# Kernel optimization log

Measured on AMD Instinct MI355X. Metric: run time of the kernel, lower is better.

## Reference

```python
import jax, jax.numpy as jnp
import numpy as np

B, S, H = 1, 2048, 1024
NH, NKV, HD = 16, 4, 64
I, E, K = 2816, 8, 2
WIN = 512
EPS = 1e-5


def setup_inputs() -> dict:
    key = jax.random.key(0)
    ks = jax.random.split(key, 8)
    sd = 0.02
    return {
        "hidden_states": jax.random.normal(ks[0], (B, S, H), jnp.float32),
        "positions": jnp.arange(S, dtype=jnp.int64),
        "w_qkv": jax.random.normal(ks[1], ((NH + 2 * NKV) * HD, H), jnp.float32) * sd,
        "w_o": jax.random.normal(ks[2], (H, NH * HD), jnp.float32) * sd,
        "router_w": jax.random.normal(ks[3], (E, H), jnp.float32) * sd,
        "ws": jax.random.normal(ks[4], (E, 2 * I, H), jnp.float32) * sd,
        "w2s": jax.random.normal(ks[5], (E, H, I), jnp.float32) * sd,
        "ln1_w": jnp.ones((H,), jnp.float32),
        "ln2_w": jnp.ones((H,), jnp.float32),
    }


def _rmsnorm(x, w):
    return x * jax.lax.rsqrt(jnp.mean(x * x, axis=-1, keepdims=True) + EPS) * w


def reference(hidden_states, positions, w_qkv, w_o, router_w, ws, w2s, ln1_w, ln2_w):
    # residual is None on entry -> residual = input, then input_layernorm
    residual = hidden_states
    x = _rmsnorm(hidden_states, ln1_w)

    # qkv projection (torch Linear: y = x @ W.T), GQA split
    qkv = jnp.einsum("bsh,oh->bso", x, w_qkv)
    q_size, kv_size = NH * HD, NKV * HD
    q = qkv[..., :q_size].reshape(B, S, NH, HD)
    k = qkv[..., q_size:q_size + kv_size].reshape(B, S, NKV, HD)
    v = qkv[..., q_size + kv_size:].reshape(B, S, NKV, HD)
    rep = NH // NKV
    k = jnp.repeat(k, rep, axis=2)  # [B,S,NH,HD]
    v = jnp.repeat(v, rep, axis=2)

    scale = HD ** -0.5
    scores = jnp.einsum("bqhd,bkhd->bhqk", q, k) * scale
    i = jnp.arange(S)[:, None]
    j = jnp.arange(S)[None, :]
    mask = (j <= i) & ((i - j) < WIN)  # causal sliding window
    scores = jnp.where(mask, scores, jnp.finfo(scores.dtype).min)
    attn = jax.nn.softmax(scores, axis=-1)
    o = jnp.einsum("bhqk,bkhd->bqhd", attn, v).reshape(B, S, NH * HD)
    attn_out = jnp.einsum("bso,ho->bsh", o, w_o)

    # pre_moe_layernorm with residual: x += residual; residual = x; x = norm(x)
    x2 = attn_out + residual
    residual2 = x2
    h = _rmsnorm(x2, ln2_w)

    # MoE: router softmax, top-k (renormalize=False), per-expert SwiGLU FFN
    t = h.reshape(-1, H)  # [T,H]
    logits = jnp.einsum("th,eh->te", t, router_w)
    probs = jax.nn.softmax(logits, axis=-1)
    vals, idx = jax.lax.top_k(probs, K)  # [T,K]
    w_dense = jnp.sum(vals[:, :, None] * jax.nn.one_hot(idx, E, dtype=t.dtype), axis=1)  # [T,E]

    out = jnp.zeros_like(t)
    for e in range(E):
        gu = jnp.einsum("th,ih->ti", t, ws[e])  # [T,2I]
        g, u = gu[:, :I], gu[:, I:]
        a = jax.nn.silu(g) * u
        y = jnp.einsum("ti,hi->th", a, w2s[e])
        out = out + w_dense[:, e:e + 1] * y

    return out.reshape(B, S, H), residual2
```

## Files before the change

kernel.cpp:

```cpp
#include <hip/hip_runtime.h>
#include <stdint.h>

typedef unsigned short u16;
typedef __attribute__((ext_vector_type(8))) short short8;
typedef __attribute__((ext_vector_type(4))) float f32x4;

constexpr int SEQ   = 2048;
constexpr int HID   = 1024;
constexpr int NHEAD = 16;
constexpr int QKVD  = 1536;
constexpr int FFI   = 2816;
constexpr int NEXP  = 8;
constexpr int WINSZ = 512;
#define EPSF 1e-5f

__device__ __forceinline__ float bf2f(u16 u) {
  union { unsigned int i; float f; } v; v.i = ((unsigned int)u) << 16; return v.f;
}
__device__ __forceinline__ u16 f2bf(float f) {
  union { unsigned int i; float f; } v; v.f = f;
  unsigned int i = v.i;
  return (u16)((i + 0x7fffu + ((i >> 16) & 1u)) >> 16);
}

__device__ __forceinline__ void gload_lds16(const void* g, void* l) {
  __builtin_amdgcn_global_load_lds((__attribute__((address_space(1))) void*)g,
                                   (__attribute__((address_space(3))) void*)l,
                                   16, 0, 0);
}

#define MFMA_BF16(a, b, c) __builtin_amdgcn_mfma_f32_16x16x32_bf16(a, b, c, 0, 0, 0)

constexpr int CN1 = QKVD * HID / 4;
constexpr int CN2 = HID * HID / 4;
constexpr int CN3 = NEXP * 2 * FFI * HID / 4;
constexpr int CN4 = NEXP * HID * FFI / 4;
constexpr int CN_SMALL = CN1 + CN2;
constexpr int CN_BIG   = CN3 + CN4;
constexpr int NCONV_BLK = CN_BIG / 1024;
constexpr int NATTN_BLK = (SEQ / 64) * NHEAD;

__global__ __launch_bounds__(256) void k_f2b_small(
    const float* __restrict__ wqkv, const float* __restrict__ wo,
    u16* __restrict__ dq, u16* __restrict__ dwo) {
  int j = (blockIdx.x * 256 + threadIdx.x) * 4;
#pragma unroll
  for (int t = 0; t < 4; ++t, ++j) {
    if (j >= CN_SMALL) return;
    const float* s; u16* d; int i = j;
    if (i < CN1) { s = wqkv; d = dq; } else { i -= CN1; s = wo; d = dwo; }
    float4 v = ((const float4*)s)[i];
    ushort4 o;
    o.x = f2bf(v.x); o.y = f2bf(v.y); o.z = f2bf(v.z); o.w = f2bf(v.w);
    ((ushort4*)d)[i] = o;
  }
}

__global__ __launch_bounds__(256) void k_rmsnorm(const float* __restrict__ x,
                                                 const float* __restrict__ w,
                                                 u16* __restrict__ y) {
  const int tkn = blockIdx.x, tid = threadIdx.x, wid = tid >> 6, lane = tid & 63;
  const float* xr = x + (size_t)tkn * HID;
  float4 v = *(const float4*)&xr[tid * 4];
  float ss = v.x * v.x + v.y * v.y + v.z * v.z + v.w * v.w;
#pragma unroll
  for (int m = 1; m < 64; m <<= 1) ss += __shfl_xor(ss, m);
  __shared__ float red[4];
  if (lane == 0) red[wid] = ss;
  __syncthreads();
  ss = red[0] + red[1] + red[2] + red[3];
  float sc = rsqrtf(ss * (1.0f / HID) + EPSF);
  float4 wv = *(const float4*)&w[tid * 4];
  ushort4 o;
  o.x = f2bf(v.x * sc * wv.x);
  o.y = f2bf(v.y * sc * wv.y);
  o.z = f2bf(v.z * sc * wv.z);
  o.w = f2bf(v.w * sc * wv.w);
  *(ushort4*)&y[(size_t)tkn * HID + tid * 4] = o;
}

__global__ __launch_bounds__(256, 2) void k_gemm_bt_sk(
    const u16* __restrict__ A, const u16* __restrict__ B, float* __restrict__ Cf,
    int N, int K, int Kc) {
  __shared__ u16 As[128 * 64];
  __shared__ u16 Bs[128 * 64];
  const int tid = threadIdx.x, wid = tid >> 6, lane = tid & 63;
  const int quad = lane >> 4, l16 = lane & 15;
  const int wr = wid >> 1, wc = wid & 1;
  const int m0 = blockIdx.y * 128, n0 = blockIdx.x * 128;
  const int M = gridDim.y * 128;
  const int kbase = blockIdx.z * Kc;
  const int sr = lane >> 3, sc = (lane & 7) * 8;
  f32x4 acc[4][4] = {};
  const int KT = Kc >> 6;
  for (int kt = 0; kt < KT; ++kt) {
    const int k0 = kbase + (kt << 6);
#pragma unroll
    for (int it = 0; it < 4; ++it) {
      int seg = wid * 4 + it;
      int row = seg * 8 + sr;
      gload_lds16(&A[(size_t)(m0 + row) * K + k0 + sc], &As[seg * 512]);
      gload_lds16(&B[(size_t)(n0 + row) * K + k0 + sc], &Bs[seg * 512]);
    }
    __syncthreads();
#pragma unroll
    for (int ks = 0; ks < 2; ++ks) {
      short8 af[4], bf[4];
#pragma unroll
      for (int t = 0; t < 4; ++t)
        af[t] = *(const short8*)&As[(64 * wr + 16 * t + l16) * 64 + ks * 32 + quad * 8];
#pragma unroll
      for (int t = 0; t < 4; ++t)
        bf[t] = *(const short8*)&Bs[(64 * wc + 16 * t + l16) * 64 + ks * 32 + quad * 8];
#pragma unroll
      for (int mt = 0; mt < 4; ++mt)
#pragma unroll
        for (int nt = 0; nt < 4; ++nt)
          acc[mt][nt] = MFMA_BF16(af[mt], bf[nt], acc[mt][nt]);
    }
    __syncthreads();
  }
  float* Co = Cf + (size_t)blockIdx.z * M * N;
#pragma unroll
  for (int mt = 0; mt < 4; ++mt)
#pragma unroll
    for (int r = 0; r < 4; ++r) {
      int row = m0 + 64 * wr + 16 * mt + quad * 4 + r;
#pragma unroll
      for (int nt = 0; nt < 4; ++nt) {
        int col = n0 + 64 * wc + 16 * nt + l16;
        Co[(size_t)row * N + col] = acc[mt][nt][r];
      }
    }
}

__global__ __launch_bounds__(256) void k_sum2_bf16(const float* __restrict__ a,
                                                   const float* __restrict__ b,
                                                   u16* __restrict__ o, int n4) {
  int i = blockIdx.x * 256 + threadIdx.x;
  if (i >= n4) return;
  float4 x = ((const float4*)a)[i];
  float4 y = ((const float4*)b)[i];
  ushort4 u;
  u.x = f2bf(x.x + y.x); u.y = f2bf(x.y + y.y);
  u.z = f2bf(x.z + y.z); u.w = f2bf(x.w + y.w);
  ((ushort4*)o)[i] = u;
}

__global__ __launch_bounds__(256, 2) void k_attn_conv(
    const u16* __restrict__ qkv, u16* __restrict__ o,
    const float* __restrict__ ws, const float* __restrict__ w2s,
    u16* __restrict__ dws, u16* __restrict__ dw2) {
  const int bid = blockIdx.x;
  const int tid = threadIdx.x;
  if (bid >= NATTN_BLK) {
    int j = (bid - NATTN_BLK) * 1024 + tid * 4;
    const float* s; u16* d;
    if (j < CN3) { s = ws; d = dws; } else { j -= CN3; s = w2s; d = dw2; }
    float4 v0 = ((const float4*)s)[j + 0];
    float4 v1 = ((const float4*)s)[j + 1];
    float4 v2 = ((const float4*)s)[j + 2];
    float4 v3 = ((const float4*)s)[j + 3];
    ushort4 o0, o1, o2, o3;
    o0.x = f2bf(v0.x); o0.y = f2bf(v0.y); o0.z = f2bf(v0.z); o0.w = f2bf(v0.w);
    o1.x = f2bf(v1.x); o1.y = f2bf(v1.y); o1.z = f2bf(v1.z); o1.w = f2bf(v1.w);
    o2.x = f2bf(v2.x); o2.y = f2bf(v2.y); o2.z = f2bf(v2.z); o2.w = f2bf(v2.w);
    o3.x = f2bf(v3.x); o3.y = f2bf(v3.y); o3.z = f2bf(v3.z); o3.w = f2bf(v3.w);
    ((ushort4*)d)[j + 0] = o0;
    ((ushort4*)d)[j + 1] = o1;
    ((ushort4*)d)[j + 2] = o2;
    ((ushort4*)d)[j + 3] = o3;
    return;
  }
  const int qb = bid & 31;
  const int h  = bid >> 5;
  const int q0 = qb * 64;
  const int g = h >> 2;
  __shared__ u16 Qs[64 * 72], Ks[64 * 72], Vt[64 * 72], Ps[64 * 72];
  const int wid = tid >> 6, lane = tid & 63;
  const int quad = lane >> 4, l16 = lane & 15;

#pragma unroll
  for (int it = 0; it < 2; ++it) {
    int idx = it * 256 + tid;
    int row = idx >> 3, c8 = (idx & 7) * 8;
    *(short8*)&Qs[row * 72 + c8] =
        *(const short8*)&qkv[(size_t)(q0 + row) * QKVD + h * 64 + c8];
  }

  f32x4 oacc[4] = {};
  float mrun[4], lrun[4];
#pragma unroll
  for (int r = 0; r < 4; ++r) { mrun[r] = -1e30f; lrun[r] = 0.f; }

  const int ktlo = (q0 >= WINSZ) ? ((q0 - WINSZ + 1) >> 6) : 0;
  const int kthi = qb;
  for (int kt = ktlo; kt <= kthi; ++kt) {
#pragma unroll
    for (int it = 0; it < 2; ++it) {
      int idx = it * 256 + tid;
      int row = idx >> 3, c8 = (idx & 7) * 8;
      *(short8*)&Ks[row * 72 + c8] =
          *(const short8*)&qkv[(size_t)(kt * 64 + row) * QKVD + 1024 + g * 64 + c8];
    }
#pragma unroll
    for (int it = 0; it < 8; ++it) {
      int idx = it * 256 + tid;
      int key = idx >> 5;
      int d = (idx & 31) * 2;
      unsigned int u = *(const unsigned int*)&qkv[(size_t)(kt * 64 + key) * QKVD + 1280 + g * 64 + d];
      Vt[d * 72 + key] = (u16)(u & 0xffffu);
      Vt[(d + 1) * 72 + key] = (u16)(u >> 16);
    }
    __syncthreads();

    f32x4 sa[4] = {};
#pragma unroll
    for (int ks = 0; ks < 2; ++ks) {
      short8 af = *(const short8*)&Qs[(16 * wid + l16) * 72 + ks * 32 + quad * 8];
#pragma unroll
      for (int ct = 0; ct < 4; ++ct) {
        short8 bf = *(const short8*)&Ks[(16 * ct + l16) * 72 + ks * 32 + quad * 8];
        sa[ct] = MFMA_BF16(af, bf, sa[ct]);
      }
    }

    float pvv[4][4];
#pragma unroll
    for (int r = 0; r < 4; ++r) {
      int i = q0 + 16 * wid + quad * 4 + r;
      float mx = -1e30f;
#pragma unroll
      for (int ct = 0; ct < 4; ++ct) {
        int j = kt * 64 + 16 * ct + l16;
        float v = sa[ct][r] * 0.125f;
        bool ok = (j <= i) && (i - j < WINSZ);
        v = ok ? v : -1e30f;
        pvv[ct][r] = v;
        mx = fmaxf(mx, v);
      }
#pragma unroll
      for (int m = 1; m < 16; m <<= 1) mx = fmaxf(mx, __shfl_xor(mx, m));
      float mnew = fmaxf(mrun[r], mx);
      float alpha = __expf(mrun[r] - mnew);
      float s = 0.f;
#pragma unroll
      for (int ct = 0; ct < 4; ++ct) {
        float p = (pvv[ct][r] > -1e29f) ? __expf(pvv[ct][r] - mnew) : 0.f;
        pvv[ct][r] = p;
        s += p;
      }
#pragma unroll
      for (int m = 1; m < 16; m <<= 1) s += __shfl_xor(s, m);
      lrun[r] = lrun[r] * alpha + s;
      mrun[r] = mnew;
#pragma unroll
      for (int ct = 0; ct < 4; ++ct) oacc[ct][r] *= alpha;
    }
#pragma unroll
    for (int ct = 0; ct < 4; ++ct)
#pragma unroll
      for (int r = 0; r < 4; ++r)
        Ps[(16 * wid + quad * 4 + r) * 72 + 16 * ct + l16] = f2bf(pvv[ct][r]);
    __syncthreads();

#pragma unroll
    for (int ks = 0; ks < 2; ++ks) {
      short8 af = *(const short8*)&Ps[(16 * wid + l16) * 72 + ks * 32 + quad * 8];
#pragma unroll
      for (int ct = 0; ct < 4; ++ct) {
        short8 bf = *(const short8*)&Vt[(16 * ct + l16) * 72 + ks * 32 + quad * 8];
        oacc[ct] = MFMA_BF16(af, bf, oacc[ct]);
      }
    }
    __syncthreads();
  }

#pragma unroll
  for (int ct = 0; ct < 4; ++ct)
#pragma unroll
    for (int r = 0; r < 4; ++r) {
      int row = q0 + 16 * wid + quad * 4 + r;
      float v = oacc[ct][r] / lrun[r];
      o[(size_t)row * HID + h * 64 + 16 * ct + l16] = f2bf(v);
    }
}

__global__ __launch_bounds__(256) void k_rms2_router(
    const float* __restrict__ o0, const float* __restrict__ o1,
    const float* __restrict__ hs, const float* __restrict__ ln2,
    const float* __restrict__ rw, float* __restrict__ out1,
    u16* __restrict__ T, int* __restrict__ counts,
    int* __restrict__ tok_idx, float* __restrict__ tok_w) {
  const int tkn = blockIdx.x, tid = threadIdx.x, wid = tid >> 6, lane = tid & 63;
  const size_t base = (size_t)tkn * HID + tid * 4;
  float4 a = *(const float4*)&o0[base];
  float4 b = *(const float4*)&o1[base];
  float4 h = *(const float4*)&hs[base];
  float4 v;
  v.x = a.x + b.x + h.x; v.y = a.y + b.y + h.y;
  v.z = a.z + b.z + h.z; v.w = a.w + b.w + h.w;
  *(float4*)&out1[base] = v;
  float ss = v.x * v.x + v.y * v.y + v.z * v.z + v.w * v.w;
#pragma unroll
  for (int m = 1; m < 64; m <<= 1) ss += __shfl_xor(ss, m);
  __shared__ float red[4];
  if (lane == 0) red[wid] = ss;
  __syncthreads();
  ss = red[0] + red[1] + red[2] + red[3];
  float sc = rsqrtf(ss * (1.0f / HID) + EPSF);
  float4 lw = *(const float4*)&ln2[tid * 4];
  float t0 = v.x * sc * lw.x;
  float t1 = v.y * sc * lw.y;
  float t2 = v.z * sc * lw.z;
  float t3 = v.w * sc * lw.w;
  ushort4 o;
  o.x = f2bf(t0); o.y = f2bf(t1); o.z = f2bf(t2); o.w = f2bf(t3);
  *(ushort4*)&T[(size_t)tkn * HID + tid * 4] = o;

  float p[8];
#pragma unroll
  for (int e = 0; e < 8; ++e) {
    float4 r = *(const float4*)&rw[e * HID + tid * 4];
    p[e] = t0 * r.x + t1 * r.y + t2 * r.z + t3 * r.w;
  }
#pragma unroll
  for (int e = 0; e < 8; ++e)
#pragma unroll
    for (int m = 1; m < 64; m <<= 1) p[e] += __shfl_xor(p[e], m);
  __shared__ float pr[4][8];
  if (lane == 0)
#pragma unroll
    for (int e = 0; e < 8; ++e) pr[wid][e] = p[e];
  __syncthreads();
  if (tid == 0) {
    float lg[8];
#pragma unroll
    for (int e = 0; e < 8; ++e) lg[e] = pr[0][e] + pr[1][e] + pr[2][e] + pr[3][e];
    float mx = lg[0];
#pragma unroll
    for (int e = 1; e < 8; ++e) mx = fmaxf(mx, lg[e]);
    float ex[8], se = 0.f;
#pragma unroll
    for (int e = 0; e < 8; ++e) { ex[e] = __expf(lg[e] - mx); se += ex[e]; }
    int b0 = 0;
#pragma unroll
    for (int e = 1; e < 8; ++e) if (lg[e] > lg[b0]) b0 = e;
    int b1 = (b0 == 0) ? 1 : 0;
#pragma unroll
    for (int e = 0; e < 8; ++e) if (e != b0 && lg[e] > lg[b1]) b1 = e;
    float inv = 1.0f / se;
    int s0 = atomicAdd(&counts[b0], 1);
    tok_idx[b0 * SEQ + s0] = tkn;
    tok_w[b0 * SEQ + s0] = ex[b0] * inv;
    int s1 = atomicAdd(&counts[b1], 1);
    tok_idx[b1 * SEQ + s1] = tkn;
    tok_w[b1 * SEQ + s1] = ex[b1] * inv;
  }
}

__global__ void k_offsets(const int* __restrict__ counts, int* __restrict__ offs) {
  if (threadIdx.x == 0 && blockIdx.x == 0) {
    int s = 0;
    for (int e = 0; e < NEXP; ++e) { offs[e] = s; s += counts[e]; }
    offs[NEXP] = s;
  }
}

__global__ __launch_bounds__(256, 2) void k_moe_gu(
    const u16* __restrict__ T, const u16* __restrict__ Wgu,
    const int* __restrict__ counts, const int* __restrict__ offs,
    const int* __restrict__ tok_idx, u16* __restrict__ Abuf) {
  const int e = blockIdx.z;
  const int cnt = counts[e];
  const int m0 = blockIdx.y * 128;
  if (m0 >= cnt) return;
  const int n0 = blockIdx.x * 64;
  const u16* We = Wgu + (size_t)e * 2 * FFI * HID;
  const int* ti = tok_idx + e * SEQ;
  const int aoff = offs[e];
  __shared__ u16 As[128 * 64], Bg[64 * 64], Bu[64 * 64];
  const int tid = threadIdx.x, wid = tid >> 6, lane = tid & 63;
  const int quad = lane >> 4, l16 = lane & 15;
  const int wr = wid >> 1, wc = wid & 1;
  const int sr = lane >> 3, sc = (lane & 7) * 8;
  int tokrow[4];
#pragma unroll
  for (int it = 0; it < 4; ++it) {
    int row = (wid * 4 + it) * 8 + sr;
    int ra = m0 + row;
    if (ra > cnt - 1) ra = cnt - 1;
    tokrow[it] = ti[ra];
  }
  f32x4 accg[4][2] = {}, accu[4][2] = {};
  for (int kt = 0; kt < 16; ++kt) {
    const int k0 = kt << 6;
#pragma unroll
    for (int it = 0; it < 4; ++it) {
      int seg = wid * 4 + it;
      gload_lds16(&T[(size_t)tokrow[it] * HID + k0 + sc], &As[seg * 512]);
    }
#pragma unroll
    for (int it = 0; it < 2; ++it) {
      int seg = wid * 2 + it;
      int row = seg * 8 + sr;
      gload_lds16(&We[(size_t)(n0 + row) * HID + k0 + sc], &Bg[seg * 512]);
      gload_lds16(&We[(size_t)(FFI + n0 + row) * HID + k0 + sc], &Bu[seg * 512]);
    }
    __syncthreads();
#pragma unroll
    for (int ks = 0; ks < 2; ++ks) {
      short8 af[4], bg[2], bu[2];
#pragma unroll
      for (int t = 0; t < 4; ++t)
        af[t] = *(const short8*)&As[(64 * wr + 16 * t + l16) * 64 + ks * 32 + quad * 8];
#pragma unroll
      for (int t = 0; t < 2; ++t) {
        bg[t] = *(const short8*)&Bg[(32 * wc + 16 * t + l16) * 64 + ks * 32 + quad * 8];
        bu[t] = *(const short8*)&Bu[(32 * wc + 16 * t + l16) * 64 + ks * 32 + quad * 8];
      }
#pragma unroll
      for (int mt = 0; mt < 4; ++mt)
#pragma unroll
        for (int nt = 0; nt < 2; ++nt) {
          accg[mt][nt] = MFMA_BF16(af[mt], bg[nt], accg[mt][nt]);
          accu[mt][nt] = MFMA_BF16(af[mt], bu[nt], accu[mt][nt]);
        }
    }
    __syncthreads();
  }
#pragma unroll
  for (int mt = 0; mt < 4; ++mt)
#pragma unroll
    for (int r = 0; r < 4; ++r) {
      int rl = 64 * wr + 16 * mt + quad * 4 + r;
      int grow = m0 + rl;
      if (grow < cnt) {
        size_t rbase = (size_t)(aoff + grow) * FFI;
#pragma unroll
        for (int nt = 0; nt < 2; ++nt) {
          int col = n0 + 32 * wc + 16 * nt + l16;
          float gv = accg[mt][nt][r];
          float uv = accu[mt][nt][r];
          float a = gv / (1.0f + __expf(-gv)) * uv;
          Abuf[rbase + col] = f2bf(a);
        }
      }
    }
}

__global__ __launch_bounds__(256, 2) void k_moe_y(
    const u16* __restrict__ Abuf, const u16* __restrict__ W2,
    const int* __restrict__ counts, const int* __restrict__ offs,
    const int* __restrict__ tok_idx, const float* __restrict__ tok_w,
    float* __restrict__ outf) {
  const int e = blockIdx.z >> 2;
  const int sk = blockIdx.z & 3;
  const int cnt = counts[e];
  const int m0 = blockIdx.y * 128;
  if (m0 >= cnt) return;
  const int n0 = blockIdx.x * 128;
  const int kbase = sk * 704;
  const u16* We = W2 + (size_t)e * HID * FFI;
  const int aoff = offs[e];
  __shared__ u16 As[128 * 64], Bs[128 * 64];
  const int tid = threadIdx.x, wid = tid >> 6, lane = tid & 63;
  const int quad = lane >> 4, l16 = lane & 15;
  const int wr = wid >> 1, wc = wid & 1;
  const int sr = lane >> 3, sc = (lane & 7) * 8;
  int arow[4];
#pragma unroll
  for (int it = 0; it < 4; ++it) {
    int row = (wid * 4 + it) * 8 + sr;
    int ra = m0 + row;
    if (ra > cnt - 1) ra = cnt - 1;
    arow[it] = aoff + ra;
  }
  f32x4 acc[4][4] = {};
  for (int kt = 0; kt < 11; ++kt) {
    const int k0 = kbase + (kt << 6);
#pragma unroll
    for (int it = 0; it < 4; ++it) {
      int seg = wid * 4 + it;
      int row = seg * 8 + sr;
      gload_lds16(&Abuf[(size_t)arow[it] * FFI + k0 + sc], &As[seg * 512]);
      gload_lds16(&We[(size_t)(n0 + row) * FFI + k0 + sc], &Bs[seg * 512]);
    }
    __syncthreads();
#pragma unroll
    for (int ks = 0; ks < 2; ++ks) {
      short8 af[4], bf[4];
#pragma unroll
      for (int t = 0; t < 4; ++t)
        af[t] = *(const short8*)&As[(64 * wr + 16 * t + l16) * 64 + ks * 32 + quad * 8];
#pragma unroll
      for (int t = 0; t < 4; ++t)
        bf[t] = *(const short8*)&Bs[(64 * wc + 16 * t + l16) * 64 + ks * 32 + quad * 8];
#pragma unroll
      for (int mt = 0; mt < 4; ++mt)
#pragma unroll
        for (int nt = 0; nt < 4; ++nt)
          acc[mt][nt] = MFMA_BF16(af[mt], bf[nt], acc[mt][nt]);
    }
    __syncthreads();
  }
#pragma unroll
  for (int mt = 0; mt < 4; ++mt)
#pragma unroll
    for (int r = 0; r < 4; ++r) {
      int rl = 64 * wr + 16 * mt + quad * 4 + r;
      int grow = m0 + rl;
      if (grow < cnt) {
        int tok = tok_idx[e * SEQ + grow];
        float wgt = tok_w[e * SEQ + grow];
        size_t obase = (size_t)tok * HID;
#pragma unroll
        for (int nt = 0; nt < 4; ++nt) {
          int col = n0 + 64 * wc + 16 * nt + l16;
          atomicAdd(&outf[obase + col], wgt * acc[mt][nt][r]);
        }
      }
    }
}

extern "C" void kernel_launch(void* const* d_in, const int* in_sizes, int n_in,
                              void* d_out, int out_size, void* d_ws, size_t ws_size,
                              hipStream_t stream) {
  const float* hs   = (const float*)d_in[0];
  const float* wqkv = (const float*)d_in[2];
  const float* wo   = (const float*)d_in[3];
  const float* rwt  = (const float*)d_in[4];
  const float* wsx  = (const float*)d_in[5];
  const float* w2s  = (const float*)d_in[6];
  const float* ln1  = (const float*)d_in[7];
  const float* ln2  = (const float*)d_in[8];
  float* out0 = (float*)d_out;
  float* out1 = out0 + (size_t)SEQ * HID;

  char* p = (char*)d_ws;
  u16* xn      = (u16*)p;   p += (size_t)SEQ * HID * 2;
  u16* qkv     = (u16*)p;   p += (size_t)SEQ * QKVD * 2;
  u16* ob      = (u16*)p;   p += (size_t)SEQ * HID * 2;
  float* qkvf  = (float*)p; p += (size_t)2 * SEQ * QKVD * 4;
  int* counts  = (int*)p;   p += 32;
  int* offs    = (int*)p;   p += 64;
  int* tok_idx = (int*)p;   p += (size_t)NEXP * SEQ * 4;
  float* tok_w = (float*)p; p += (size_t)NEXP * SEQ * 4;
  u16* abuf    = (u16*)p;   p += (size_t)2 * SEQ * FFI * 2;
  u16* wqkv_b  = (u16*)p;   p += (size_t)QKVD * HID * 2;
  u16* wo_b    = (u16*)p;   p += (size_t)HID * HID * 2;
  u16* ws_b    = (u16*)p;   p += (size_t)NEXP * 2 * FFI * HID * 2;
  u16* w2s_b   = (u16*)p;   p += (size_t)NEXP * HID * FFI * 2;

  u16* tb      = xn;
  float* oacc0 = qkvf;
  float* oacc1 = qkvf + (size_t)SEQ * HID;

  hipMemsetAsync(counts, 0, 32, stream);
  hipMemsetAsync(out0, 0, (size_t)SEQ * HID * 4, stream);

  k_f2b_small<<<(CN_SMALL / 4 + 255) / 256, 256, 0, stream>>>(
      wqkv, wo, wqkv_b, wo_b);
  k_rmsnorm<<<SEQ, 256, 0, stream>>>(hs, ln1, xn);
  k_gemm_bt_sk<<<dim3(QKVD / 128, SEQ / 128, 2), 256, 0, stream>>>(
      xn, wqkv_b, qkvf, QKVD, HID, 512);
  k_sum2_bf16<<<(SEQ * QKVD / 4 + 255) / 256, 256, 0, stream>>>(
      qkvf, qkvf + (size_t)SEQ * QKVD, qkv, SEQ * QKVD / 4);
  k_attn_conv<<<NATTN_BLK + NCONV_BLK, 256, 0, stream>>>(
      qkv, ob, wsx, w2s, ws_b, w2s_b);
  k_gemm_bt_sk<<<dim3(HID / 128, SEQ / 128, 2), 256, 0, stream>>>(
      ob, wo_b, oacc0, HID, HID, 512);
  k_rms2_router<<<SEQ, 256, 0, stream>>>(oacc0, oacc1, hs, ln2, rwt, out1, tb,
                                         counts, tok_idx, tok_w);
  k_offsets<<<1, 64, 0, stream>>>(counts, offs);
  k_moe_gu<<<dim3(FFI / 64, SEQ / 128, NEXP), 256, 0, stream>>>(
      tb, ws_b, counts, offs, tok_idx, abuf);
  k_moe_y<<<dim3(HID / 128, SEQ / 128, NEXP * 4), 256, 0, stream>>>(
      abuf, w2s_b, counts, offs, tok_idx, tok_w, out0);
}
```

Baseline: 634.6 us.

## Double-buffer GEMM tiles, drop split-K for dense GEMMs, replace MoE atomics with gather

Fuses the first RMSNorm with the small weight conversion into one launch. The dense QKV and output-projection GEMMs drop split-K and the separate reduction kernel in favour of 128x64 tiles that write bf16 or fp32 directly. All GEMM kernels (dense, MoE gate/up, MoE down) now double-buffer their LDS tiles so global loads overlap MFMA work. The MoE down projection cuts split-K from 4 to 2, writes partials into a per-slot buffer, and a new gather kernel combines the two experts per token with their routing weights. This removes the output memset and the float atomics, at the cost of more LDS per block and an extra fp32 intermediate buffer plus one more launch.

```diff
diff --git a/kernel.cpp b/kernel.cpp
--- a/kernel.cpp
+++ b/kernel.cpp
@@ -14,9 +14,6 @@
 constexpr int WINSZ = 512;
 #define EPSF 1e-5f
 
-__device__ __forceinline__ float bf2f(u16 u) {
-  union { unsigned int i; float f; } v; v.i = ((unsigned int)u) << 16; return v.f;
-}
 __device__ __forceinline__ u16 f2bf(float f) {
   union { unsigned int i; float f; } v; v.f = f;
   unsigned int i = v.i;
@@ -40,14 +37,37 @@
 constexpr int NCONV_BLK = CN_BIG / 1024;
 constexpr int NATTN_BLK = (SEQ / 64) * NHEAD;
 
-__global__ __launch_bounds__(256) void k_f2b_small(
+__global__ __launch_bounds__(256) void k_prep(
+    const float* __restrict__ x, const float* __restrict__ w, u16* __restrict__ y,
     const float* __restrict__ wqkv, const float* __restrict__ wo,
     u16* __restrict__ dq, u16* __restrict__ dwo) {
-  int j = (blockIdx.x * 256 + threadIdx.x) * 4;
-#pragma unroll
-  for (int t = 0; t < 4; ++t, ++j) {
-    if (j >= CN_SMALL) return;
-    const float* s; u16* d; int i = j;
+  const int bid = blockIdx.x, tid = threadIdx.x;
+  __shared__ float red[4];
+  if (bid < SEQ) {
+    const int wid = tid >> 6, lane = tid & 63;
+    const float* xr = x + (size_t)bid * HID;
+    float4 v = *(const float4*)&xr[tid * 4];
+    float ss = v.x * v.x + v.y * v.y + v.z * v.z + v.w * v.w;
+#pragma unroll
+    for (int m = 1; m < 64; m <<= 1) ss += __shfl_xor(ss, m);
+    if (lane == 0) red[wid] = ss;
+    __syncthreads();
+    ss = red[0] + red[1] + red[2] + red[3];
+    float sc = rsqrtf(ss * (1.0f / HID) + EPSF);
+    float4 wv = *(const float4*)&w[tid * 4];
+    ushort4 o;
+    o.x = f2bf(v.x * sc * wv.x);
+    o.y = f2bf(v.y * sc * wv.y);
+    o.z = f2bf(v.z * sc * wv.z);
+    o.w = f2bf(v.w * sc * wv.w);
+    *(ushort4*)&y[(size_t)bid * HID + tid * 4] = o;
+    return;
+  }
+  int j = (bid - SEQ) * 1024 + tid;
+#pragma unroll
+  for (int t = 0; t < 4; ++t) {
+    int i = j + t * 256;
+    const float* s; u16* d;
     if (i < CN1) { s = wqkv; d = dq; } else { i -= CN1; s = wo; d = dwo; }
     float4 v = ((const float4*)s)[i];
     ushort4 o;
@@ -56,95 +76,84 @@
   }
 }
 
-__global__ __launch_bounds__(256) void k_rmsnorm(const float* __restrict__ x,
-                                                 const float* __restrict__ w,
-                                                 u16* __restrict__ y) {
-  const int tkn = blockIdx.x, tid = threadIdx.x, wid = tid >> 6, lane = tid & 63;
-  const float* xr = x + (size_t)tkn * HID;
-  float4 v = *(const float4*)&xr[tid * 4];
-  float ss = v.x * v.x + v.y * v.y + v.z * v.z + v.w * v.w;
-#pragma unroll
-  for (int m = 1; m < 64; m <<= 1) ss += __shfl_xor(ss, m);
-  __shared__ float red[4];
-  if (lane == 0) red[wid] = ss;
-  __syncthreads();
-  ss = red[0] + red[1] + red[2] + red[3];
-  float sc = rsqrtf(ss * (1.0f / HID) + EPSF);
-  float4 wv = *(const float4*)&w[tid * 4];
-  ushort4 o;
-  o.x = f2bf(v.x * sc * wv.x);
-  o.y = f2bf(v.y * sc * wv.y);
-  o.z = f2bf(v.z * sc * wv.z);
-  o.w = f2bf(v.w * sc * wv.w);
-  *(ushort4*)&y[(size_t)tkn * HID + tid * 4] = o;
-}
-
-__global__ __launch_bounds__(256, 2) void k_gemm_bt_sk(
-    const u16* __restrict__ A, const u16* __restrict__ B, float* __restrict__ Cf,
-    int N, int K, int Kc) {
-  __shared__ u16 As[128 * 64];
-  __shared__ u16 Bs[128 * 64];
+__global__ __launch_bounds__(256, 2) void k_gemm_bt(
+    const u16* __restrict__ A, const u16* __restrict__ B,
+    void* __restrict__ Cout, int N, int K, int wf32) {
+  __shared__ u16 As[2][128 * 64];
+  __shared__ u16 Bs[2][64 * 64];
   const int tid = threadIdx.x, wid = tid >> 6, lane = tid & 63;
   const int quad = lane >> 4, l16 = lane & 15;
   const int wr = wid >> 1, wc = wid & 1;
-  const int m0 = blockIdx.y * 128, n0 = blockIdx.x * 128;
-  const int M = gridDim.y * 128;
-  const int kbase = blockIdx.z * Kc;
+  const int m0 = blockIdx.y * 128, n0 = blockIdx.x * 64;
   const int sr = lane >> 3, sc = (lane & 7) * 8;
-  f32x4 acc[4][4] = {};
-  const int KT = Kc >> 6;
+  f32x4 acc[4][2] = {};
+  const int KT = K >> 6;
+
+#define GSTAGE(buf, k0)                                                          \
+  {                                                                              \
+    _Pragma("unroll") for (int it = 0; it < 4; ++it) {                           \
+      int seg = wid * 4 + it;                                                    \
+      int row = seg * 8 + sr;                                                    \
+      gload_lds16(&A[(size_t)(m0 + row) * K + (k0) + sc], &As[buf][seg * 512]);  \
+    }                                                                            \
+    _Pragma("unroll") for (int it = 0; it < 2; ++it) {                           \
+      int seg = wid * 2 + it;                                                    \
+      int row = seg * 8 + sr;                                                    \
+      gload_lds16(&B[(size_t)(n0 + row) * K + (k0) + sc], &Bs[buf][seg * 512]);  \
+    }                                                                            \
+  }
+
+  GSTAGE(0, 0);
+  __syncthreads();
+  int cur = 0;
   for (int kt = 0; kt < KT; ++kt) {
-    const int k0 = kbase + (kt << 6);
-#pragma unroll
-    for (int it = 0; it < 4; ++it) {
-      int seg = wid * 4 + it;
-      int row = seg * 8 + sr;
-      gload_lds16(&A[(size_t)(m0 + row) * K + k0 + sc], &As[seg * 512]);
-      gload_lds16(&B[(size_t)(n0 + row) * K + k0 + sc], &Bs[seg * 512]);
+    if (kt + 1 < KT) GSTAGE(cur ^ 1, (kt + 1) << 6);
+#pragma unroll
+    for (int ks = 0; ks < 2; ++ks) {
+      short8 af[4], bf[2];
+#pragma unroll
+      for (int t = 0; t < 4; ++t)
+        af[t] = *(const short8*)&As[cur][(64 * wr + 16 * t + l16) * 64 + ks * 32 + quad * 8];
+#pragma unroll
+      for (int t = 0; t < 2; ++t)
+        bf[t] = *(const short8*)&Bs[cur][(32 * wc + 16 * t + l16) * 64 + ks * 32 + quad * 8];
+#pragma unroll
+      for (int mt = 0; mt < 4; ++mt)
+#pragma unroll
+        for (int nt = 0; nt < 2; ++nt)
+          acc[mt][nt] = MFMA_BF16(af[mt], bf[nt], acc[mt][nt]);
     }
     __syncthreads();
-#pragma unroll
-    for (int ks = 0; ks < 2; ++ks) {
-      short8 af[4], bf[4];
-#pragma unroll
-      for (int t = 0; t < 4; ++t)
-        af[t] = *(const short8*)&As[(64 * wr + 16 * t + l16) * 64 + ks * 32 + quad * 8];
-#pragma unroll
-      for (int t = 0; t < 4; ++t)
-        bf[t] = *(const short8*)&Bs[(64 * wc + 16 * t + l16) * 64 + ks * 32 + quad * 8];
-#pragma unroll
-      for (int mt = 0; mt < 4; ++mt)
-#pragma unroll
-        for (int nt = 0; nt < 4; ++nt)
-          acc[mt][nt] = MFMA_BF16(af[mt], bf[nt], acc[mt][nt]);
-    }
-    __syncthreads();
-  }
-  float* Co = Cf + (size_t)blockIdx.z * M * N;
-#pragma unroll
-  for (int mt = 0; mt < 4; ++mt)
-#pragma unroll
-    for (int r = 0; r < 4; ++r) {
-      int row = m0 + 64 * wr + 16 * mt + quad * 4 + r;
-#pragma unroll
-      for (int nt = 0; nt < 4; ++nt) {
-        int col = n0 + 64 * wc + 16 * nt + l16;
-        Co[(size_t)row * N + col] = acc[mt][nt][r];
-      }
-    }
-}
-
-__global__ __launch_bounds__(256) void k_sum2_bf16(const float* __restrict__ a,
-                                                   const float* __restrict__ b,
-                                                   u16* __restrict__ o, int n4) {
-  int i = blockIdx.x * 256 + threadIdx.x;
-  if (i >= n4) return;
-  float4 x = ((const float4*)a)[i];
-  float4 y = ((const float4*)b)[i];
-  ushort4 u;
-  u.x = f2bf(x.x + y.x); u.y = f2bf(x.y + y.y);
-  u.z = f2bf(x.z + y.z); u.w = f2bf(x.w + y.w);
-  ((ushort4*)o)[i] = u;
+    cur ^= 1;
+  }
+#undef GSTAGE
+  if (wf32) {
+    float* C = (float*)Cout;
+#pragma unroll
+    for (int mt = 0; mt < 4; ++mt)
+#pragma unroll
+      for (int r = 0; r < 4; ++r) {
+        int row = m0 + 64 * wr + 16 * mt + quad * 4 + r;
+#pragma unroll
+        for (int nt = 0; nt < 2; ++nt) {
+          int col = n0 + 32 * wc + 16 * nt + l16;
+          C[(size_t)row * N + col] = acc[mt][nt][r];
+        }
+      }
+  } else {
+    u16* C = (u16*)Cout;
+#pragma unroll
+    for (int mt = 0; mt < 4; ++mt)
+#pragma unroll
+      for (int r = 0; r < 4; ++r) {
+        int row = m0 + 64 * wr + 16 * mt + quad * 4 + r;
+#pragma unroll
+        for (int nt = 0; nt < 2; ++nt) {
+          int col = n0 + 32 * wc + 16 * nt + l16;
+          C[(size_t)row * N + col] = f2bf(acc[mt][nt][r]);
+        }
+      }
+  }
 }
 
 __global__ __launch_bounds__(256, 2) void k_attn_conv(
@@ -154,22 +163,17 @@
   const int bid = blockIdx.x;
   const int tid = threadIdx.x;
   if (bid >= NATTN_BLK) {
-    int j = (bid - NATTN_BLK) * 1024 + tid * 4;
-    const float* s; u16* d;
-    if (j < CN3) { s = ws; d = dws; } else { j -= CN3; s = w2s; d = dw2; }
-    float4 v0 = ((const float4*)s)[j + 0];
-    float4 v1 = ((const float4*)s)[j + 1];
-    float4 v2 = ((const float4*)s)[j + 2];
-    float4 v3 = ((const float4*)s)[j + 3];
-    ushort4 o0, o1, o2, o3;
-    o0.x = f2bf(v0.x); o0.y = f2bf(v0.y); o0.z = f2bf(v0.z); o0.w = f2bf(v0.w);
-    o1.x = f2bf(v1.x); o1.y = f2bf(v1.y); o1.z = f2bf(v1.z); o1.w = f2bf(v1.w);
-    o2.x = f2bf(v2.x); o2.y = f2bf(v2.y); o2.z = f2bf(v2.z); o2.w = f2bf(v2.w);
-    o3.x = f2bf(v3.x); o3.y = f2bf(v3.y); o3.z = f2bf(v3.z); o3.w = f2bf(v3.w);
-    ((ushort4*)d)[j + 0] = o0;
-    ((ushort4*)d)[j + 1] = o1;
-    ((ushort4*)d)[j + 2] = o2;
-    ((ushort4*)d)[j + 3] = o3;
+    int j = (bid - NATTN_BLK) * 1024 + tid;
+#pragma unroll
+    for (int t = 0; t < 4; ++t) {
+      int i = j + t * 256;
+      const float* s; u16* d;
+      if (i < CN3) { s = ws; d = dws; } else { i -= CN3; s = w2s; d = dw2; }
+      float4 v = ((const float4*)s)[i];
+      ushort4 u;
+      u.x = f2bf(v.x); u.y = f2bf(v.y); u.z = f2bf(v.z); u.w = f2bf(v.w);
+      ((ushort4*)d)[i] = u;
+    }
     return;
   }
   const int qb = bid & 31;
@@ -287,19 +291,17 @@
 }
 
 __global__ __launch_bounds__(256) void k_rms2_router(
-    const float* __restrict__ o0, const float* __restrict__ o1,
-    const float* __restrict__ hs, const float* __restrict__ ln2,
-    const float* __restrict__ rw, float* __restrict__ out1,
-    u16* __restrict__ T, int* __restrict__ counts,
-    int* __restrict__ tok_idx, float* __restrict__ tok_w) {
+    const float* __restrict__ of, const float* __restrict__ hs,
+    const float* __restrict__ ln2, const float* __restrict__ rw,
+    float* __restrict__ out1, u16* __restrict__ T, int* __restrict__ counts,
+    int* __restrict__ tok_idx, int* __restrict__ tok_slot,
+    float* __restrict__ tok_pw) {
   const int tkn = blockIdx.x, tid = threadIdx.x, wid = tid >> 6, lane = tid & 63;
   const size_t base = (size_t)tkn * HID + tid * 4;
-  float4 a = *(const float4*)&o0[base];
-  float4 b = *(const float4*)&o1[base];
+  float4 a = *(const float4*)&of[base];
   float4 h = *(const float4*)&hs[base];
   float4 v;
-  v.x = a.x + b.x + h.x; v.y = a.y + b.y + h.y;
-  v.z = a.z + b.z + h.z; v.w = a.w + b.w + h.w;
+  v.x = a.x + h.x; v.y = a.y + h.y; v.z = a.z + h.z; v.w = a.w + h.w;
   *(float4*)&out1[base] = v;
   float ss = v.x * v.x + v.y * v.y + v.z * v.z + v.w * v.w;
 #pragma unroll
@@ -352,10 +354,12 @@
     float inv = 1.0f / se;
     int s0 = atomicAdd(&counts[b0], 1);
     tok_idx[b0 * SEQ + s0] = tkn;
-    tok_w[b0 * SEQ + s0] = ex[b0] * inv;
+    tok_slot[2 * tkn] = b0 * SEQ + s0;
+    tok_pw[2 * tkn] = ex[b0] * inv;
     int s1 = atomicAdd(&counts[b1], 1);
     tok_idx[b1 * SEQ + s1] = tkn;
-    tok_w[b1 * SEQ + s1] = ex[b1] * inv;
+    tok_slot[2 * tkn + 1] = b1 * SEQ + s1;
+    tok_pw[2 * tkn + 1] = ex[b1] * inv;
   }
 }
 
@@ -379,7 +383,7 @@
   const u16* We = Wgu + (size_t)e * 2 * FFI * HID;
   const int* ti = tok_idx + e * SEQ;
   const int aoff = offs[e];
-  __shared__ u16 As[128 * 64], Bg[64 * 64], Bu[64 * 64];
+  __shared__ u16 As[2][128 * 64], Bg[2][64 * 64], Bu[2][64 * 64];
   const int tid = threadIdx.x, wid = tid >> 6, lane = tid & 63;
   const int quad = lane >> 4, l16 = lane & 15;
   const int wr = wid >> 1, wc = wid & 1;
@@ -393,31 +397,37 @@
     tokrow[it] = ti[ra];
   }
   f32x4 accg[4][2] = {}, accu[4][2] = {};
+
+#define MSTAGE(buf, k0)                                                            \
+  {                                                                                \
+    _Pragma("unroll") for (int it = 0; it < 4; ++it) {                             \
+      int seg = wid * 4 + it;                                                      \
+      gload_lds16(&T[(size_t)tokrow[it] * HID + (k0) + sc], &As[buf][seg * 512]);  \
+    }                                                                              \
+    _Pragma("unroll") for (int it = 0; it < 2; ++it) {                             \
+      int seg = wid * 2 + it;                                                      \
+      int row = seg * 8 + sr;                                                      \
+      gload_lds16(&We[(size_t)(n0 + row) * HID + (k0) + sc], &Bg[buf][seg * 512]); \
+      gload_lds16(&We[(size_t)(FFI + n0 + row) * HID + (k0) + sc],                 \
+                  &Bu[buf][seg * 512]);                                            \
+    }                                                                              \
+  }
+
+  MSTAGE(0, 0);
+  __syncthreads();
+  int cur = 0;
   for (int kt = 0; kt < 16; ++kt) {
-    const int k0 = kt << 6;
-#pragma unroll
-    for (int it = 0; it < 4; ++it) {
-      int seg = wid * 4 + it;
-      gload_lds16(&T[(size_t)tokrow[it] * HID + k0 + sc], &As[seg * 512]);
-    }
-#pragma unroll
-    for (int it = 0; it < 2; ++it) {
-      int seg = wid * 2 + it;
-      int row = seg * 8 + sr;
-      gload_lds16(&We[(size_t)(n0 + row) * HID + k0 + sc], &Bg[seg * 512]);
-      gload_lds16(&We[(size_t)(FFI + n0 + row) * HID + k0 + sc], &Bu[seg * 512]);
-    }
-    __syncthreads();
+    if (kt + 1 < 16) MSTAGE(cur ^ 1, (kt + 1) << 6);
 #pragma unroll
     for (int ks = 0; ks < 2; ++ks) {
       short8 af[4], bg[2], bu[2];
 #pragma unroll
       for (int t = 0; t < 4; ++t)
-        af[t] = *(const short8*)&As[(64 * wr + 16 * t + l16) * 64 + ks * 32 + quad * 8];
+        af[t] = *(const short8*)&As[cur][(64 * wr + 16 * t + l16) * 64 + ks * 32 + quad * 8];
 #pragma unroll
       for (int t = 0; t < 2; ++t) {
-        bg[t] = *(const short8*)&Bg[(32 * wc + 16 * t + l16) * 64 + ks * 32 + quad * 8];
-        bu[t] = *(const short8*)&Bu[(32 * wc + 16 * t + l16) * 64 + ks * 32 + quad * 8];
+        bg[t] = *(const short8*)&Bg[cur][(32 * wc + 16 * t + l16) * 64 + ks * 32 + quad * 8];
+        bu[t] = *(const short8*)&Bu[cur][(32 * wc + 16 * t + l16) * 64 + ks * 32 + quad * 8];
       }
 #pragma unroll
       for (int mt = 0; mt < 4; ++mt)
@@ -428,7 +438,9 @@
         }
     }
     __syncthreads();
-  }
+    cur ^= 1;
+  }
+#undef MSTAGE
 #pragma unroll
   for (int mt = 0; mt < 4; ++mt)
 #pragma unroll
@@ -452,18 +464,17 @@
 __global__ __launch_bounds__(256, 2) void k_moe_y(
     const u16* __restrict__ Abuf, const u16* __restrict__ W2,
     const int* __restrict__ counts, const int* __restrict__ offs,
-    const int* __restrict__ tok_idx, const float* __restrict__ tok_w,
-    float* __restrict__ outf) {
-  const int e = blockIdx.z >> 2;
-  const int sk = blockIdx.z & 3;
+    float* __restrict__ ybuf) {
+  const int e = blockIdx.z >> 1;
+  const int sk = blockIdx.z & 1;
   const int cnt = counts[e];
   const int m0 = blockIdx.y * 128;
   if (m0 >= cnt) return;
   const int n0 = blockIdx.x * 128;
-  const int kbase = sk * 704;
+  const int kbase = sk * 1408;
   const u16* We = W2 + (size_t)e * HID * FFI;
   const int aoff = offs[e];
-  __shared__ u16 As[128 * 64], Bs[128 * 64];
+  __shared__ u16 As[2][128 * 64], Bs[2][128 * 64];
   const int tid = threadIdx.x, wid = tid >> 6, lane = tid & 63;
   const int quad = lane >> 4, l16 = lane & 15;
   const int wr = wid >> 1, wc = wid & 1;
@@ -477,25 +488,31 @@
     arow[it] = aoff + ra;
   }
   f32x4 acc[4][4] = {};
-  for (int kt = 0; kt < 11; ++kt) {
-    const int k0 = kbase + (kt << 6);
-#pragma unroll
-    for (int it = 0; it < 4; ++it) {
-      int seg = wid * 4 + it;
-      int row = seg * 8 + sr;
-      gload_lds16(&Abuf[(size_t)arow[it] * FFI + k0 + sc], &As[seg * 512]);
-      gload_lds16(&We[(size_t)(n0 + row) * FFI + k0 + sc], &Bs[seg * 512]);
-    }
-    __syncthreads();
+
+#define YSTAGE(buf, k0)                                                             \
+  {                                                                                 \
+    _Pragma("unroll") for (int it = 0; it < 4; ++it) {                              \
+      int seg = wid * 4 + it;                                                       \
+      int row = seg * 8 + sr;                                                       \
+      gload_lds16(&Abuf[(size_t)arow[it] * FFI + (k0) + sc], &As[buf][seg * 512]);  \
+      gload_lds16(&We[(size_t)(n0 + row) * FFI + (k0) + sc], &Bs[buf][seg * 512]);  \
+    }                                                                               \
+  }
+
+  YSTAGE(0, kbase);
+  __syncthreads();
+  int cur = 0;
+  for (int kt = 0; kt < 22; ++kt) {
+    if (kt + 1 < 22) YSTAGE(cur ^ 1, kbase + ((kt + 1) << 6));
 #pragma unroll
     for (int ks = 0; ks < 2; ++ks) {
       short8 af[4], bf[4];
 #pragma unroll
       for (int t = 0; t < 4; ++t)
-        af[t] = *(const short8*)&As[(64 * wr + 16 * t + l16) * 64 + ks * 32 + quad * 8];
+        af[t] = *(const short8*)&As[cur][(64 * wr + 16 * t + l16) * 64 + ks * 32 + quad * 8];
 #pragma unroll
       for (int t = 0; t < 4; ++t)
-        bf[t] = *(const short8*)&Bs[(64 * wc + 16 * t + l16) * 64 + ks * 32 + quad * 8];
+        bf[t] = *(const short8*)&Bs[cur][(64 * wc + 16 * t + l16) * 64 + ks * 32 + quad * 8];
 #pragma unroll
       for (int mt = 0; mt < 4; ++mt)
 #pragma unroll
@@ -503,7 +520,10 @@
           acc[mt][nt] = MFMA_BF16(af[mt], bf[nt], acc[mt][nt]);
     }
     __syncthreads();
-  }
+    cur ^= 1;
+  }
+#undef YSTAGE
+  float* Y = ybuf + (size_t)sk * 2 * SEQ * HID;
 #pragma unroll
   for (int mt = 0; mt < 4; ++mt)
 #pragma unroll
@@ -511,16 +531,37 @@
       int rl = 64 * wr + 16 * mt + quad * 4 + r;
       int grow = m0 + rl;
       if (grow < cnt) {
-        int tok = tok_idx[e * SEQ + grow];
-        float wgt = tok_w[e * SEQ + grow];
-        size_t obase = (size_t)tok * HID;
+        size_t obase = (size_t)(aoff + grow) * HID;
 #pragma unroll
         for (int nt = 0; nt < 4; ++nt) {
           int col = n0 + 64 * wc + 16 * nt + l16;
-          atomicAdd(&outf[obase + col], wgt * acc[mt][nt][r]);
+          Y[obase + col] = acc[mt][nt][r];
         }
       }
     }
+}
+
+__global__ __launch_bounds__(256) void k_moe_out(
+    const float* __restrict__ yb, const int* __restrict__ offs,
+    const int* __restrict__ tok_slot, const float* __restrict__ tok_pw,
+    float* __restrict__ out0) {
+  const int t = blockIdx.x, tid = threadIdx.x;
+  const int v0 = tok_slot[2 * t], v1 = tok_slot[2 * t + 1];
+  const float w0 = tok_pw[2 * t], w1 = tok_pw[2 * t + 1];
+  const size_t g0 = (size_t)(offs[v0 >> 11] + (v0 & (SEQ - 1))) * HID;
+  const size_t g1 = (size_t)(offs[v1 >> 11] + (v1 & (SEQ - 1))) * HID;
+  const size_t YP = (size_t)2 * SEQ * HID;
+  const int c = tid * 4;
+  float4 a0 = *(const float4*)&yb[g0 + c];
+  float4 b0 = *(const float4*)&yb[YP + g0 + c];
+  float4 a1 = *(const float4*)&yb[g1 + c];
+  float4 b1 = *(const float4*)&yb[YP + g1 + c];
+  float4 r;
+  r.x = w0 * (a0.x + b0.x) + w1 * (a1.x + b1.x);
+  r.y = w0 * (a0.y + b0.y) + w1 * (a1.y + b1.y);
+  r.z = w0 * (a0.z + b0.z) + w1 * (a1.z + b1.z);
+  r.w = w0 * (a0.w + b0.w) + w1 * (a1.w + b1.w);
+  *(float4*)&out0[(size_t)t * HID + c] = r;
 }
 
 extern "C" void kernel_launch(void* const* d_in, const int* in_sizes, int n_in,
@@ -538,43 +579,40 @@
   float* out1 = out0 + (size_t)SEQ * HID;
 
   char* p = (char*)d_ws;
-  u16* xn      = (u16*)p;   p += (size_t)SEQ * HID * 2;
-  u16* qkv     = (u16*)p;   p += (size_t)SEQ * QKVD * 2;
-  u16* ob      = (u16*)p;   p += (size_t)SEQ * HID * 2;
-  float* qkvf  = (float*)p; p += (size_t)2 * SEQ * QKVD * 4;
-  int* counts  = (int*)p;   p += 32;
-  int* offs    = (int*)p;   p += 64;
-  int* tok_idx = (int*)p;   p += (size_t)NEXP * SEQ * 4;
-  float* tok_w = (float*)p; p += (size_t)NEXP * SEQ * 4;
-  u16* abuf    = (u16*)p;   p += (size_t)2 * SEQ * FFI * 2;
-  u16* wqkv_b  = (u16*)p;   p += (size_t)QKVD * HID * 2;
-  u16* wo_b    = (u16*)p;   p += (size_t)HID * HID * 2;
-  u16* ws_b    = (u16*)p;   p += (size_t)NEXP * 2 * FFI * HID * 2;
-  u16* w2s_b   = (u16*)p;   p += (size_t)NEXP * HID * FFI * 2;
-
-  u16* tb      = xn;
-  float* oacc0 = qkvf;
-  float* oacc1 = qkvf + (size_t)SEQ * HID;
+  u16* xn       = (u16*)p;   p += (size_t)SEQ * HID * 2;
+  u16* qkv      = (u16*)p;   p += (size_t)SEQ * QKVD * 2;
+  u16* ob       = (u16*)p;   p += (size_t)SEQ * HID * 2;
+  float* of     = (float*)p; p += (size_t)SEQ * HID * 4;
+  int* counts   = (int*)p;   p += 32;
+  int* offs     = (int*)p;   p += 64;
+  int* tok_idx  = (int*)p;   p += (size_t)NEXP * SEQ * 4;
+  int* tok_slot = (int*)p;   p += (size_t)2 * SEQ * 4;
+  float* tok_pw = (float*)p; p += (size_t)2 * SEQ * 4;
+  u16* abuf     = (u16*)p;   p += (size_t)2 * SEQ * FFI * 2;
+  float* ybuf   = (float*)p; p += (size_t)2 * 2 * SEQ * HID * 4;
+  u16* wqkv_b   = (u16*)p;   p += (size_t)QKVD * HID * 2;
+  u16* wo_b     = (u16*)p;   p += (size_t)HID * HID * 2;
+  u16* ws_b     = (u16*)p;   p += (size_t)NEXP * 2 * FFI * HID * 2;
+  u16* w2s_b    = (u16*)p;   p += (size_t)NEXP * HID * FFI * 2;
+
+  u16* tb = xn;
 
   hipMemsetAsync(counts, 0, 32, stream);
-  hipMemsetAsync(out0, 0, (size_t)SEQ * HID * 4, stream);
-
-  k_f2b_small<<<(CN_SMALL / 4 + 255) / 256, 256, 0, stream>>>(
-      wqkv, wo, wqkv_b, wo_b);
-  k_rmsnorm<<<SEQ, 256, 0, stream>>>(hs, ln1, xn);
-  k_gemm_bt_sk<<<dim3(QKVD / 128, SEQ / 128, 2), 256, 0, stream>>>(
-      xn, wqkv_b, qkvf, QKVD, HID, 512);
-  k_sum2_bf16<<<(SEQ * QKVD / 4 + 255) / 256, 256, 0, stream>>>(
-      qkvf, qkvf + (size_t)SEQ * QKVD, qkv, SEQ * QKVD / 4);
+
+  k_prep<<<SEQ + CN_SMALL / 1024, 256, 0, stream>>>(
+      hs, ln1, xn, wqkv, wo, wqkv_b, wo_b);
+  k_gemm_bt<<<dim3(QKVD / 64, SEQ / 128), 256, 0, stream>>>(
+      xn, wqkv_b, qkv, QKVD, HID, 0);
   k_attn_conv<<<NATTN_BLK + NCONV_BLK, 256, 0, stream>>>(
       qkv, ob, wsx, w2s, ws_b, w2s_b);
-  k_gemm_bt_sk<<<dim3(HID / 128, SEQ / 128, 2), 256, 0, stream>>>(
-      ob, wo_b, oacc0, HID, HID, 512);
-  k_rms2_router<<<SEQ, 256, 0, stream>>>(oacc0, oacc1, hs, ln2, rwt, out1, tb,
-                                         counts, tok_idx, tok_w);
+  k_gemm_bt<<<dim3(HID / 64, SEQ / 128), 256, 0, stream>>>(
+      ob, wo_b, of, HID, HID, 1);
+  k_rms2_router<<<SEQ, 256, 0, stream>>>(of, hs, ln2, rwt, out1, tb,
+                                         counts, tok_idx, tok_slot, tok_pw);
   k_offsets<<<1, 64, 0, stream>>>(counts, offs);
   k_moe_gu<<<dim3(FFI / 64, SEQ / 128, NEXP), 256, 0, stream>>>(
       tb, ws_b, counts, offs, tok_idx, abuf);
-  k_moe_y<<<dim3(HID / 128, SEQ / 128, NEXP * 4), 256, 0, stream>>>(
-      abuf, w2s_b, counts, offs, tok_idx, tok_w, out0);
-}
+  k_moe_y<<<dim3(HID / 128, SEQ / 128, NEXP * 2), 256, 0, stream>>>(
+      abuf, w2s_b, counts, offs, ybuf);
+  k_moe_out<<<SEQ, 256, 0, stream>>>(ybuf, offs, tok_slot, tok_pw, out0);
+}
```

After: 692.1 us. +9.1%, slower.
